# Optimization experiments

Measured on AMD Instinct MI355X. Metric: run time of the kernel, lower is better.

## Reference

```python
import jax, jax.numpy as jnp
import numpy as np

MAX_VAL = 10000.0
KS = (1, 5, 10, 20, 50)
B, V, L = 256, 128000, 200


def setup_inputs() -> dict:
    key = jax.random.key(0)
    k1, k2, k3 = jax.random.split(key, 3)
    scores = jax.random.normal(k1, (B, V), dtype=jnp.float32)
    labels = jax.random.randint(k2, (B,), 0, V, dtype=jnp.int64)
    seqs = jax.random.randint(k3, (B, L), 0, V, dtype=jnp.int64)
    return {"scores": scores, "labels": labels, "seqs": seqs}


def reference(scores, labels, seqs):
    b = scores.shape[0]
    rows = jnp.arange(b)
    # gather predicted score for the true label BEFORE masking (torch order)
    predicts = scores[rows, labels]  # [B]
    # scatter -MAX_VAL at history items (masked scatter)
    masked = scores.at[rows[:, None], seqs].set(-MAX_VAL)  # [B, V]
    valid_length = (masked > -MAX_VAL).sum(-1).astype(jnp.float32)  # [B]
    rank = (predicts[:, None] < masked).sum(-1).astype(jnp.float32)  # [B]
    res = []
    for k in KS:
        indicator = (rank < k).astype(jnp.float32)
        res.append((indicator / jnp.log2(rank + 2.0)).mean())  # NDCG@k
        res.append(indicator.mean())  # Recall@k
    res.append((1.0 / (rank + 1.0)).mean())  # MRR
    res.append((1.0 - rank / valid_length).mean())  # AUC-like
    res.append(jnp.float32(0.0))
    return jnp.stack(res)
```

## Files before the change

### kernel.cpp

```cpp
#include <hip/hip_runtime.h>
#include <math.h>

#define B_CONST 256
#define V_CONST 128000
#define L_CONST 200
#define SLICES  8


__global__ __launch_bounds__(256) void rank_count_kernel(
    const float* __restrict__ scores,
    const int* __restrict__ labels,
    const int* __restrict__ seqs,
    int* __restrict__ partial,
    int* __restrict__ subp,
    int* __restrict__ distp)
{
    const int slice = blockIdx.x;
    const int b     = blockIdx.y;
    const int tid   = threadIdx.x;
    const int wave  = tid >> 6;

    const float* row  = scores + (size_t)b * V_CONST;
    const float4* row4 = (const float4*)row;
    const float predict = row[labels[b]];

    const int base = slice * 4000 + tid;
    int cnt = 0;

    {
        float4 v0 = row4[base];
        float4 v1 = row4[base + 1 * 256];
        float4 v2 = row4[base + 2 * 256];
        float4 v3 = row4[base + 3 * 256];
        float4 v4 = row4[base + 4 * 256];
        float4 v5 = row4[base + 5 * 256];
        float4 v6 = row4[base + 6 * 256];
        float4 v7 = row4[base + 7 * 256];
        cnt += (v0.x > predict) + (v0.y > predict) + (v0.z > predict) + (v0.w > predict);
        cnt += (v1.x > predict) + (v1.y > predict) + (v1.z > predict) + (v1.w > predict);
        cnt += (v2.x > predict) + (v2.y > predict) + (v2.z > predict) + (v2.w > predict);
        cnt += (v3.x > predict) + (v3.y > predict) + (v3.z > predict) + (v3.w > predict);
        cnt += (v4.x > predict) + (v4.y > predict) + (v4.z > predict) + (v4.w > predict);
        cnt += (v5.x > predict) + (v5.y > predict) + (v5.z > predict) + (v5.w > predict);
        cnt += (v6.x > predict) + (v6.y > predict) + (v6.z > predict) + (v6.w > predict);
        cnt += (v7.x > predict) + (v7.y > predict) + (v7.z > predict) + (v7.w > predict);
    }
    {
        float4 v0 = row4[base + 8  * 256];
        float4 v1 = row4[base + 9  * 256];
        float4 v2 = row4[base + 10 * 256];
        float4 v3 = row4[base + 11 * 256];
        float4 v4 = row4[base + 12 * 256];
        float4 v5 = row4[base + 13 * 256];
        float4 v6 = row4[base + 14 * 256];
        if (tid < 160) {
            float4 v7 = row4[slice * 4000 + 3840 + tid];
            cnt += (v7.x > predict) + (v7.y > predict) + (v7.z > predict) + (v7.w > predict);
        }
        cnt += (v0.x > predict) + (v0.y > predict) + (v0.z > predict) + (v0.w > predict);
        cnt += (v1.x > predict) + (v1.y > predict) + (v1.z > predict) + (v1.w > predict);
        cnt += (v2.x > predict) + (v2.y > predict) + (v2.z > predict) + (v2.w > predict);
        cnt += (v3.x > predict) + (v3.y > predict) + (v3.z > predict) + (v3.w > predict);
        cnt += (v4.x > predict) + (v4.y > predict) + (v4.z > predict) + (v4.w > predict);
        cnt += (v5.x > predict) + (v5.y > predict) + (v5.z > predict) + (v5.w > predict);
        cnt += (v6.x > predict) + (v6.y > predict) + (v6.z > predict) + (v6.w > predict);
    }

    #pragma unroll
    for (int off = 32; off > 0; off >>= 1)
        cnt += __shfl_down(cnt, off, 64);
    if ((tid & 63) == 0)
        partial[(b * SLICES + slice) * 4 + wave] = cnt;

    if (slice == 0) {
        int dflag = 0, sflag = 0;
        if (tid < L_CONST) {
            const int* srow = seqs + b * L_CONST;
            const int s = srow[tid];
            bool first = true;
            for (int j = 0; j < tid; ++j)
                if (srow[j] == s) { first = false; break; }
            if (first) {
                dflag = 1;
                sflag = (row[s] > predict) ? 1 : 0;
            }
        }
        #pragma unroll
        for (int off = 32; off > 0; off >>= 1) {
            dflag += __shfl_down(dflag, off, 64);
            sflag += __shfl_down(sflag, off, 64);
        }
        if ((tid & 63) == 0) {
            distp[b * 4 + wave] = dflag;
            subp [b * 4 + wave] = sflag;
        }
    }
}

__global__ __launch_bounds__(256) void finalize_kernel(
    const int* __restrict__ partial,
    const int* __restrict__ subp,
    const int* __restrict__ distp,
    float* __restrict__ out)
{
    const int b = threadIdx.x;
    int gt = 0;
    #pragma unroll
    for (int s = 0; s < SLICES * 4; ++s) gt += partial[b * SLICES * 4 + s];
    int sub = 0, dist = 0;
    #pragma unroll
    for (int w = 0; w < 4; ++w) { sub += subp[b * 4 + w]; dist += distp[b * 4 + w]; }

    const float rank  = (float)(gt - sub);
    const float valid = (float)(V_CONST - dist);

    const float ks[5] = {1.0f, 5.0f, 10.0f, 20.0f, 50.0f};
    float vals[12];
    const float invlog = 1.0f / log2f(rank + 2.0f);
    #pragma unroll
    for (int i = 0; i < 5; ++i) {
        const float ind = (rank < ks[i]) ? 1.0f : 0.0f;
        vals[2 * i]     = ind * invlog;
        vals[2 * i + 1] = ind;
    }
    vals[10] = 1.0f / (rank + 1.0f);
    vals[11] = 1.0f - rank / valid;

    __shared__ float red[4];
    for (int q = 0; q < 12; ++q) {
        float v = vals[q];
        #pragma unroll
        for (int off = 32; off > 0; off >>= 1)
            v += __shfl_down(v, off, 64);
        if ((b & 63) == 0) red[b >> 6] = v;
        __syncthreads();
        if (b == 0) out[q] = (red[0] + red[1] + red[2] + red[3]) * (1.0f / B_CONST);
        __syncthreads();
    }
    if (b == 0) out[12] = 0.0f;
}

extern "C" void kernel_launch(void* const* d_in, const int* in_sizes, int n_in,
                              void* d_out, int out_size, void* d_ws, size_t ws_size,
                              hipStream_t stream) {
    const float* scores = (const float*)d_in[0];
    const int*   labels = (const int*)d_in[1];
    const int*   seqs   = (const int*)d_in[2];
    float* out = (float*)d_out;
    int*   ws  = (int*)d_ws;

    int* partial = ws;
    int* subp    = ws + B_CONST * SLICES * 4;
    int* distp   = ws + B_CONST * SLICES * 4 + B_CONST * 4;

    rank_count_kernel<<<dim3(SLICES, B_CONST), 256, 0, stream>>>(
        scores, labels, seqs, partial, subp, distp);
    finalize_kernel<<<1, 256, 0, stream>>>(partial, subp, distp, out);
}
```

Baseline: 242.7 us.

## Stream score rows through LDS with async global_load_lds multi-buffer pipeline

```diff
diff --git a/kernel.cpp b/kernel.cpp
--- a/kernel.cpp
+++ b/kernel.cpp
@@ -4,8 +4,18 @@
 #define B_CONST 256
 #define V_CONST 128000
 #define L_CONST 200
-#define SLICES  8
+#define SLICES  5
+#define NTILES  25
+#define NBUF    4
 
+
+__device__ __forceinline__ void load_lds16(const float* g, float4* l) {
+    __builtin_amdgcn_global_load_lds(
+        (const __attribute__((address_space(1))) void*)g,
+        (__attribute__((address_space(3))) void*)l, 16, 0, 0);
+}
+
+#define WAITV(n) asm volatile("s_waitcnt vmcnt(" #n ")" ::: "memory")
 
 __global__ __launch_bounds__(256) void rank_count_kernel(
     const float* __restrict__ scores,
@@ -18,71 +28,55 @@
     const int slice = blockIdx.x;
     const int b     = blockIdx.y;
     const int tid   = threadIdx.x;
-    const int wave  = tid >> 6;
+    const int w     = tid >> 6;
+    const int lane  = tid & 63;
 
-    const float* row  = scores + (size_t)b * V_CONST;
-    const float4* row4 = (const float4*)row;
+    __shared__ float4 buf[NBUF][256];
+    __shared__ int s_seq[L_CONST];
+
+    const float* row = scores + (size_t)b * V_CONST;
     const float predict = row[labels[b]];
+    if (slice == 0 && tid < L_CONST) s_seq[tid] = seqs[b * L_CONST + tid];
+    __syncthreads();
 
-    const int base = slice * 4000 + tid;
+    const float* chunk = row + slice * (V_CONST / SLICES);
+
+#define FILL(t) load_lds16(chunk + (t) * 1024 + w * 256 + lane * 4, \
+                           &buf[(t) & (NBUF - 1)][w * 64])
+
     int cnt = 0;
+#define COUNT(t) do { \
+        float4 v = buf[(t) & (NBUF - 1)][w * 64 + lane]; \
+        cnt += (v.x > predict) + (v.y > predict) + (v.z > predict) + (v.w > predict); \
+    } while (0)
 
-    {
-        float4 v0 = row4[base];
-        float4 v1 = row4[base + 1 * 256];
-        float4 v2 = row4[base + 2 * 256];
-        float4 v3 = row4[base + 3 * 256];
-        float4 v4 = row4[base + 4 * 256];
-        float4 v5 = row4[base + 5 * 256];
-        float4 v6 = row4[base + 6 * 256];
-        float4 v7 = row4[base + 7 * 256];
-        cnt += (v0.x > predict) + (v0.y > predict) + (v0.z > predict) + (v0.w > predict);
-        cnt += (v1.x > predict) + (v1.y > predict) + (v1.z > predict) + (v1.w > predict);
-        cnt += (v2.x > predict) + (v2.y > predict) + (v2.z > predict) + (v2.w > predict);
-        cnt += (v3.x > predict) + (v3.y > predict) + (v3.z > predict) + (v3.w > predict);
-        cnt += (v4.x > predict) + (v4.y > predict) + (v4.z > predict) + (v4.w > predict);
-        cnt += (v5.x > predict) + (v5.y > predict) + (v5.z > predict) + (v5.w > predict);
-        cnt += (v6.x > predict) + (v6.y > predict) + (v6.z > predict) + (v6.w > predict);
-        cnt += (v7.x > predict) + (v7.y > predict) + (v7.z > predict) + (v7.w > predict);
+    FILL(0); FILL(1); FILL(2);
+    for (int t = 0; t < NTILES - 3; ++t) {
+        FILL(t + 3);
+        WAITV(3);
+        COUNT(t);
     }
-    {
-        float4 v0 = row4[base + 8  * 256];
-        float4 v1 = row4[base + 9  * 256];
-        float4 v2 = row4[base + 10 * 256];
-        float4 v3 = row4[base + 11 * 256];
-        float4 v4 = row4[base + 12 * 256];
-        float4 v5 = row4[base + 13 * 256];
-        float4 v6 = row4[base + 14 * 256];
-        if (tid < 160) {
-            float4 v7 = row4[slice * 4000 + 3840 + tid];
-            cnt += (v7.x > predict) + (v7.y > predict) + (v7.z > predict) + (v7.w > predict);
-        }
-        cnt += (v0.x > predict) + (v0.y > predict) + (v0.z > predict) + (v0.w > predict);
-        cnt += (v1.x > predict) + (v1.y > predict) + (v1.z > predict) + (v1.w > predict);
-        cnt += (v2.x > predict) + (v2.y > predict) + (v2.z > predict) + (v2.w > predict);
-        cnt += (v3.x > predict) + (v3.y > predict) + (v3.z > predict) + (v3.w > predict);
-        cnt += (v4.x > predict) + (v4.y > predict) + (v4.z > predict) + (v4.w > predict);
-        cnt += (v5.x > predict) + (v5.y > predict) + (v5.z > predict) + (v5.w > predict);
-        cnt += (v6.x > predict) + (v6.y > predict) + (v6.z > predict) + (v6.w > predict);
-    }
+    WAITV(2); COUNT(NTILES - 3);
+    WAITV(1); COUNT(NTILES - 2);
+    WAITV(0); COUNT(NTILES - 1);
 
     #pragma unroll
     for (int off = 32; off > 0; off >>= 1)
         cnt += __shfl_down(cnt, off, 64);
-    if ((tid & 63) == 0)
-        partial[(b * SLICES + slice) * 4 + wave] = cnt;
+    if (lane == 0)
+        partial[(b * SLICES + slice) * 4 + w] = cnt;
 
     if (slice == 0) {
         int dflag = 0, sflag = 0;
         if (tid < L_CONST) {
-            const int* srow = seqs + b * L_CONST;
-            const int s = srow[tid];
+            const int s = s_seq[tid];
+            const float sv = row[s];
             bool first = true;
             for (int j = 0; j < tid; ++j)
-                if (srow[j] == s) { first = false; break; }
+                if (s_seq[j] == s) { first = false; break; }
             if (first) {
                 dflag = 1;
-                sflag = (row[s] > predict) ? 1 : 0;
+                sflag = (sv > predict) ? 1 : 0;
             }
         }
         #pragma unroll
@@ -90,9 +84,9 @@
             dflag += __shfl_down(dflag, off, 64);
             sflag += __shfl_down(sflag, off, 64);
         }
-        if ((tid & 63) == 0) {
-            distp[b * 4 + wave] = dflag;
-            subp [b * 4 + wave] = sflag;
+        if (lane == 0) {
+            distp[b * 4 + w] = dflag;
+            subp [b * 4 + w] = sflag;
         }
     }
 }
```

Result: faster. 204.3 us (-15.8%).
